# Kernel optimization log

Hardware: AMD Instinct MI355X
Metric: run time of the kernel (lower is better)

## Reference

```python
import jax, jax.numpy as jnp
import numpy as np

T, B = 128, 512
OBS_DIM = 512
HIDDEN = 512
ACTION_DIM = 18
LN_EPS = 1e-6  # flax LayerNorm default


def _layer_norm(x, scale, bias):
    m = jnp.mean(x, axis=-1, keepdims=True)
    v = jnp.var(x, axis=-1, keepdims=True)
    return (x - m) * jax.lax.rsqrt(v + LN_EPS) * scale + bias


def setup_inputs() -> dict:
    key = jax.random.key(0)
    ks = jax.random.split(key, 16)
    sc = lambda k, sh: jax.random.normal(k, sh, jnp.float32) * (1.0 / np.sqrt(sh[0]))
    d = {}
    d['hidden'] = jax.random.normal(ks[0], (B, HIDDEN), jnp.float32)
    d['obs'] = jax.random.normal(ks[1], (T, B, OBS_DIM), jnp.float32)
    d['dones'] = jax.random.randint(ks[2], (T, B), 0, 2).astype(bool)
    d['last_acts'] = jax.random.randint(ks[3], (T, B), 0, ACTION_DIM, dtype=jnp.int32)
    in0 = OBS_DIM + ACTION_DIM
    d['w0'] = sc(ks[4], (in0, HIDDEN)); d['b0'] = jnp.zeros((HIDDEN,), jnp.float32)
    d['ln0_s'] = jnp.ones((HIDDEN,), jnp.float32); d['ln0_b'] = jnp.zeros((HIDDEN,), jnp.float32)
    d['w1'] = sc(ks[5], (HIDDEN, HIDDEN)); d['b1'] = jnp.zeros((HIDDEN,), jnp.float32)
    d['ln1_s'] = jnp.ones((HIDDEN,), jnp.float32); d['ln1_b'] = jnp.zeros((HIDDEN,), jnp.float32)
    d['w_ir'] = sc(ks[6], (HIDDEN, HIDDEN)); d['b_ir'] = jnp.zeros((HIDDEN,), jnp.float32)
    d['w_iz'] = sc(ks[7], (HIDDEN, HIDDEN)); d['b_iz'] = jnp.zeros((HIDDEN,), jnp.float32)
    d['w_in'] = sc(ks[8], (HIDDEN, HIDDEN)); d['b_in'] = jnp.zeros((HIDDEN,), jnp.float32)
    d['w_hr'] = sc(ks[9], (HIDDEN, HIDDEN))
    d['w_hz'] = sc(ks[10], (HIDDEN, HIDDEN))
    d['w_hn'] = sc(ks[11], (HIDDEN, HIDDEN)); d['b_hn'] = jnp.zeros((HIDDEN,), jnp.float32)
    d['w_out'] = sc(ks[12], (HIDDEN, ACTION_DIM)); d['b_out'] = jnp.zeros((ACTION_DIM,), jnp.float32)
    return d


def reference(hidden, obs, dones, last_acts,
              w0, b0, ln0_s, ln0_b, w1, b1, ln1_s, ln1_b,
              w_ir, b_ir, w_iz, b_iz, w_in, b_in,
              w_hr, w_hz, w_hn, b_hn, w_out, b_out):
    # embed last actions and concat with obs: [T, B, obs_dim + action_dim]
    one_hot = jax.nn.one_hot(last_acts, ACTION_DIM, dtype=obs.dtype)
    x = jnp.concatenate([obs, one_hot], axis=-1)
    # MLP encoder: Dense -> LayerNorm -> relu, applied over all (T, B) at once
    x = jax.nn.relu(_layer_norm(x @ w0 + b0, ln0_s, ln0_b))
    x = jax.nn.relu(_layer_norm(x @ w1 + b1, ln1_s, ln1_b))

    # ScannedRNN: GRUCell with reset-to-zero carry on done, scanned over time
    def step(h, xs):
        xt, dt = xs  # xt: [B, H], dt: [B] bool
        h = jnp.where(dt[:, None], jnp.zeros_like(h), h)
        r = jax.nn.sigmoid(xt @ w_ir + b_ir + h @ w_hr)
        z = jax.nn.sigmoid(xt @ w_iz + b_iz + h @ w_hz)
        n = jnp.tanh(xt @ w_in + b_in + r * (h @ w_hn + b_hn))
        h_new = (1.0 - z) * n + z * h
        return h_new, h_new

    new_hidden, y = jax.lax.scan(step, hidden, (x, dones))
    q_vals = y @ w_out + b_out  # [T, B, action_dim]
    return new_hidden, q_vals
```

## Files before the change

kernel.cpp:

```cpp
#include <hip/hip_runtime.h>
#include <cstdint>
#include <cstddef>


#define TT 128
#define BBATCH 512
#define HH 512
#define MM 65536
#define AD 18

typedef __attribute__((ext_vector_type(8))) short short8;
typedef __attribute__((ext_vector_type(4))) float float4v;
typedef __attribute__((ext_vector_type(4))) unsigned int uint4v;

__device__ __forceinline__ unsigned short f2bf(float f) {
  union { float f; unsigned int u; } v; v.f = f;
  unsigned int r = v.u + 0x7fffu + ((v.u >> 16) & 1u);
  return (unsigned short)(r >> 16);
}
__device__ __forceinline__ float bf2f(unsigned short h) {
  union { unsigned int u; float f; } v; v.u = ((unsigned int)h) << 16;
  return v.f;
}

__device__ __forceinline__ unsigned int load_u32_coh(const unsigned int* p) {
  unsigned int v;
  asm volatile("global_load_dword %0, %1, off sc0 sc1\n\ts_waitcnt vmcnt(0)"
               : "=v"(v) : "v"(p) : "memory");
  return v;
}
__device__ __forceinline__ void store_u32_coh(unsigned int* p, unsigned int v) {
  asm volatile("global_store_dword %0, %1, off sc0 sc1"
               :: "v"(p), "v"(v) : "memory");
}
__device__ __forceinline__ void store_u16_coh(unsigned short* p, unsigned int v) {
  asm volatile("global_store_short %0, %1, off sc0 sc1"
               :: "v"(p), "v"(v) : "memory");
}

typedef __attribute__((address_space(3))) unsigned int* lds_u32p;
typedef const __attribute__((address_space(1))) unsigned int* glb_u32p;
__device__ __forceinline__ void async16(void* lds, const void* g) {
  __builtin_amdgcn_global_load_lds(
      (glb_u32p)(unsigned long long)g,
      (lds_u32p)(unsigned int)(unsigned long long)lds, 16, 0, 0);
}


__global__ __launch_bounds__(256) void k_conv_obs(
    const float* __restrict__ src, unsigned short* __restrict__ dst,
    unsigned int* __restrict__ flag) {
  if (blockIdx.x == 0 && threadIdx.x == 0) *flag = 0u;
  int i = blockIdx.x * 256 + threadIdx.x;
  float4v v = ((const float4v*)src)[i];
  unsigned long long pk = (unsigned long long)f2bf(v[0])
      | ((unsigned long long)f2bf(v[1]) << 16)
      | ((unsigned long long)f2bf(v[2]) << 32)
      | ((unsigned long long)f2bf(v[3]) << 48);
  ((unsigned long long*)dst)[i] = pk;
}

__global__ __launch_bounds__(256) void k_prep_t(
    const float* __restrict__ w0, const float* __restrict__ w1,
    const float* __restrict__ wir, const float* __restrict__ wiz,
    const float* __restrict__ win,
    unsigned short* __restrict__ W0at, unsigned short* __restrict__ W1t,
    unsigned short* __restrict__ Wit) {
  int o = blockIdx.x * 256 + threadIdx.x;
  int n = o >> 9, k = o & 511;
  int z = blockIdx.y;
  const float* s = (z == 0) ? w0 : (z == 1) ? w1 : (z == 2) ? wir
                 : (z == 3) ? wiz : win;
  unsigned short b = f2bf(s[k * 512 + n]);
  if (z == 0) W0at[o] = b;
  else if (z == 1) W1t[o] = b;
  else Wit[(size_t)(z - 2) * 262144 + o] = b;
}

__global__ __launch_bounds__(256) void k_prep_whf(
    const float* __restrict__ whr, const float* __restrict__ whz,
    const float* __restrict__ whn, unsigned short* __restrict__ Whf) {
  int i = blockIdx.x * 256 + threadIdx.x;
  int k = i / 1536, n = i - k * 1536;
  const float* s = (n < 512) ? whr : (n < 1024) ? whz : whn;
  float v = s[k * 512 + (n & 511)];
  Whf[((size_t)(k >> 3) * 1536 + n) * 8 + (k & 7)] = f2bf(v);
}

__global__ __launch_bounds__(256) void k_prep_misc(
    const float* __restrict__ w0, const float* __restrict__ bir,
    const float* __restrict__ biz, const float* __restrict__ bin,
    const float* __restrict__ wout, const float* __restrict__ hidden,
    const int* __restrict__ dI,
    unsigned short* __restrict__ w0act, float* __restrict__ gib,
    unsigned short* __restrict__ WoutT, unsigned short* __restrict__ hbuf,
    unsigned int* __restrict__ ready, unsigned int* __restrict__ flag) {
  int i = blockIdx.x * 256 + threadIdx.x;
  if (i < 9216) {
    int a = i >> 9, n = i & 511;
    w0act[i] = f2bf(w0[(512 + a) * 512 + n]);
  }
  if (i < 1536)
    gib[i] = (i < 512) ? bir[i] : (i < 1024) ? biz[i - 512] : bin[i - 1024];
  if (i < 32768) {
    int n = i >> 9, k = i & 511;
    WoutT[i] = f2bf(n < AD ? wout[k * AD + n] : 0.f);
  }
  if (i < 262144) hbuf[i] = f2bf(hidden[i]);
  if (i < 33280) ready[i] = 0u;
  if (i < 16384) { if (dI[i] & 0xFFFFFFFE) atomicOr(flag, 1u); }
}


template <int MODE>
__global__ __launch_bounds__(256) void k_gemm_bt(
    const unsigned short* __restrict__ Ab,
    const unsigned short* __restrict__ Btb,
    unsigned short* __restrict__ Cb,
    int Ndim, const float* __restrict__ bias,
    const unsigned short* __restrict__ gW,
    const int* __restrict__ acts) {
  __shared__ unsigned short As[4096];
  __shared__ unsigned short Bs[4096];
  const int tid = threadIdx.x, wave = tid >> 6, lane = tid & 63;
  const int quad = lane >> 4, l15 = lane & 15;
  const int m0 = blockIdx.x * 128, n0 = blockIdx.y * 128;
  const int mblk = (wave & 1) * 64, nblk = (wave >> 1) * 64;

  float4v acc[4][4];
#pragma unroll
  for (int a = 0; a < 4; ++a)
#pragma unroll
    for (int b = 0; b < 4; ++b) acc[a][b] = (float4v){0.f, 0.f, 0.f, 0.f};

  for (int k0 = 0; k0 < 512; k0 += 32) {
#pragma unroll
    for (int r = 0; r < 2; ++r) {
      int u = r * 256 + wave * 64 + lane;
      int ch = u >> 7, mm = u & 127;
      async16(&As[(size_t)(r * 256 + wave * 64) * 8],
              Ab + (size_t)(m0 + mm) * 512 + k0 + ch * 8);
      async16(&Bs[(size_t)(r * 256 + wave * 64) * 8],
              Btb + (size_t)(n0 + mm) * 512 + k0 + ch * 8);
    }
    __syncthreads();
    short8 afr[4], bfr[4];
#pragma unroll
    for (int mi = 0; mi < 4; ++mi)
      afr[mi] = *(const short8*)&As[((quad << 7) + mblk + mi * 16 + l15) * 8];
#pragma unroll
    for (int ni = 0; ni < 4; ++ni)
      bfr[ni] = *(const short8*)&Bs[((quad << 7) + nblk + ni * 16 + l15) * 8];
#pragma unroll
    for (int mi = 0; mi < 4; ++mi)
#pragma unroll
      for (int ni = 0; ni < 4; ++ni)
        acc[mi][ni] = __builtin_amdgcn_mfma_f32_16x16x32_bf16(
            afr[mi], bfr[ni], acc[mi][ni], 0, 0, 0);
    __syncthreads();
  }

#pragma unroll
  for (int mi = 0; mi < 4; ++mi) {
#pragma unroll
    for (int i = 0; i < 4; ++i) {
      int row = m0 + mblk + mi * 16 + quad * 4 + i;
      int arow = (MODE == 1) ? acts[row] : 0;
#pragma unroll
      for (int ni = 0; ni < 4; ++ni) {
        int col = n0 + nblk + ni * 16 + l15;
        float v = acc[mi][ni][i] + bias[col];
        if (MODE == 1) v += bf2f(gW[arow * 512 + col]);
        Cb[(size_t)row * Ndim + col] = f2bf(v);
      }
    }
  }
}


__global__ __launch_bounds__(256) void k_ln_relu(
    const unsigned short* __restrict__ X, unsigned short* __restrict__ Y,
    const float* __restrict__ sc, const float* __restrict__ bi) {
  int row = blockIdx.x * 4 + (threadIdx.x >> 6);
  int lane = threadIdx.x & 63;
  uint4v u = *(const uint4v*)(X + (size_t)row * 512 + lane * 8);
  float v[8];
#pragma unroll
  for (int j = 0; j < 4; ++j) {
    v[2 * j] = bf2f((unsigned short)(u[j] & 0xffffu));
    v[2 * j + 1] = bf2f((unsigned short)(u[j] >> 16));
  }
  float s = 0.f, q = 0.f;
#pragma unroll
  for (int j = 0; j < 8; ++j) { s += v[j]; q += v[j] * v[j]; }
#pragma unroll
  for (int d = 1; d < 64; d <<= 1) {
    s += __shfl_xor(s, d, 64);
    q += __shfl_xor(q, d, 64);
  }
  float mean = s * (1.f / 512.f);
  float var = fmaxf(q * (1.f / 512.f) - mean * mean, 0.f);
  float rstd = rsqrtf(var + 1e-6f);
  float4v s0 = *(const float4v*)(sc + lane * 8);
  float4v s1 = *(const float4v*)(sc + lane * 8 + 4);
  float4v c0 = *(const float4v*)(bi + lane * 8);
  float4v c1 = *(const float4v*)(bi + lane * 8 + 4);
  uint4v w;
#pragma unroll
  for (int j = 0; j < 4; ++j) {
    float a0 = fmaxf((v[2 * j] - mean) * rstd * (j < 2 ? s0[2 * j] : s1[2 * j - 4])
                         + (j < 2 ? c0[2 * j] : c1[2 * j - 4]), 0.f);
    float a1 = fmaxf((v[2 * j + 1] - mean) * rstd
                         * (j < 2 ? s0[2 * j + 1] : s1[2 * j - 3])
                         + (j < 2 ? c0[2 * j + 1] : c1[2 * j - 3]), 0.f);
    w[j] = (unsigned int)f2bf(a0) | ((unsigned int)f2bf(a1) << 16);
  }
  *(uint4v*)(Y + (size_t)row * 512 + lane * 8) = w;
}


__global__ __launch_bounds__(256, 1) void k_gru(
    const unsigned short* __restrict__ Whf, const unsigned short* __restrict__ gin,
    const float* __restrict__ bhn, const int* __restrict__ dI,
    const unsigned char* __restrict__ dB, const unsigned int* __restrict__ flag,
    const unsigned short* __restrict__ hbuf, unsigned short* __restrict__ ybuf,
    float* __restrict__ outh, unsigned int* __restrict__ ready) {
  const int tid = threadIdx.x, wave = tid >> 6, lane = tid & 63;
  const int quad = lane >> 4, l15 = lane & 15;
  const int rt = blockIdx.x & 7;
  const int cc = blockIdx.x >> 3;
  const int r0 = rt * 64 + wave * 16;
  const int col = cc * 16 + l15;
  const int bytemode = (int)(*flag);
  const float bhn_c = bhn[col];

  short8 bw[3][16];
#pragma unroll
  for (int kc = 0; kc < 16; ++kc)
#pragma unroll
    for (int g = 0; g < 3; ++g) {
      size_t u = (size_t)(kc * 4 + quad) * 1536 + (g * 512 + col);
      bw[g][kc] = *(const short8*)(Whf + u * 8);
    }

  float hprev[4];
#pragma unroll
  for (int i = 0; i < 4; ++i) {
    int row = r0 + quad * 4 + i;
    hprev[i] = bf2f(hbuf[(size_t)row * 512 + col]);
  }

  const int myrowA = r0 + l15;

  float ginr[4], ginz[4], ginn[4];
  int dd[4], dA;
  {
    const unsigned short* gbase = gin;
#pragma unroll
    for (int i = 0; i < 4; ++i) {
      int row = r0 + quad * 4 + i;
      dd[i] = bytemode ? (int)dB[row] : dI[row];
      ginr[i] = bf2f(gbase[(size_t)row * 1536 + col]);
      ginz[i] = bf2f(gbase[(size_t)row * 1536 + 512 + col]);
      ginn[i] = bf2f(gbase[(size_t)row * 1536 + 1024 + col]);
    }
    dA = bytemode ? (int)dB[myrowA] : dI[myrowA];
  }

  for (int t = 0; t < TT; ++t) {
    if (t > 0) {
      if (wave == 0) {
        const unsigned int* fp =
            ready + ((size_t)rt * 130 + t) * 32 + (lane & 31);
        unsigned int v;
        int guard = 0;
        do {
          v = load_u32_coh(fp);
        } while (__ballot(v == 0u) != 0ull && ++guard < (1 << 22));
      }
      __syncthreads();
      asm volatile("" ::: "memory");
    }

    const unsigned short* hsrc =
        (t == 0) ? hbuf : ybuf + (size_t)(t - 1) * 262144;
    const unsigned short* ap = hsrc + (size_t)myrowA * 512 + quad * 8;
    short8 af[16];
#pragma unroll
    for (int kc = 0; kc < 16; ++kc) af[kc] = *(const short8*)(ap + kc * 32);
    if (dA) {
      const short8 z8 = {0, 0, 0, 0, 0, 0, 0, 0};
#pragma unroll
      for (int kc = 0; kc < 16; ++kc) af[kc] = z8;
    }

    float4v a0 = {0.f, 0.f, 0.f, 0.f}, a1 = a0, a2 = a0;
#pragma unroll
    for (int kc = 0; kc < 16; ++kc) {
      a0 = __builtin_amdgcn_mfma_f32_16x16x32_bf16(af[kc], bw[0][kc], a0, 0, 0, 0);
      a1 = __builtin_amdgcn_mfma_f32_16x16x32_bf16(af[kc], bw[1][kc], a1, 0, 0, 0);
      a2 = __builtin_amdgcn_mfma_f32_16x16x32_bf16(af[kc], bw[2][kc], a2, 0, 0, 0);
    }

    unsigned short* ydst = ybuf + (size_t)t * 262144;
#pragma unroll
    for (int i = 0; i < 4; ++i) {
      int row = r0 + quad * 4 + i;
      float hold = dd[i] ? 0.f : hprev[i];
      float r = 1.f / (1.f + __expf(-(a0[i] + ginr[i])));
      float z = 1.f / (1.f + __expf(-(a1[i] + ginz[i])));
      float npre = ginn[i] + r * (a2[i] + bhn_c);
      float n = 1.f - 2.f / (1.f + __expf(2.f * npre));
      float hnew = (1.f - z) * n + z * hold;
      hprev[i] = hnew;
      store_u16_coh(ydst + (size_t)row * 512 + col, (unsigned int)f2bf(hnew));
      if (t == TT - 1) outh[(size_t)row * 512 + col] = hnew;
    }

    __syncthreads();
    if (tid == 0)
      store_u32_coh(&ready[((size_t)rt * 130 + t + 1) * 32 + cc], 1u);

    if (t < TT - 1) {
      int tn = t + 1;
      const unsigned short* gbase = gin + (size_t)tn * 512 * 1536;
#pragma unroll
      for (int i = 0; i < 4; ++i) {
        int row = r0 + quad * 4 + i;
        dd[i] = bytemode ? (int)dB[tn * 512 + row] : dI[tn * 512 + row];
        ginr[i] = bf2f(gbase[(size_t)row * 1536 + col]);
        ginz[i] = bf2f(gbase[(size_t)row * 1536 + 512 + col]);
        ginn[i] = bf2f(gbase[(size_t)row * 1536 + 1024 + col]);
      }
      dA = bytemode ? (int)dB[tn * 512 + myrowA] : dI[tn * 512 + myrowA];
    }
  }
}


__global__ __launch_bounds__(256) void k_qout(
    const unsigned short* __restrict__ Yb, const unsigned short* __restrict__ Wt,
    const float* __restrict__ bout, float* __restrict__ Q) {
  __shared__ unsigned short As[4096];
  __shared__ unsigned short Bs[2048];
  const int tid = threadIdx.x, wave = tid >> 6, lane = tid & 63;
  const int quad = lane >> 4, l15 = lane & 15;
  const int m0 = blockIdx.x * 128;

  float4v acc[2][4];
#pragma unroll
  for (int a = 0; a < 2; ++a)
#pragma unroll
    for (int b = 0; b < 4; ++b) acc[a][b] = (float4v){0.f, 0.f, 0.f, 0.f};

  for (int k0 = 0; k0 < 512; k0 += 32) {
#pragma unroll
    for (int r = 0; r < 2; ++r) {
      int u = r * 256 + wave * 64 + lane;
      int ch = u >> 7, mm = u & 127;
      async16(&As[(size_t)(r * 256 + wave * 64) * 8],
              Yb + (size_t)(m0 + mm) * 512 + k0 + ch * 8);
    }
    {
      int u = wave * 64 + lane;
      int ch = u >> 6, nn = u & 63;
      async16(&Bs[(size_t)(wave * 64) * 8], Wt + (size_t)nn * 512 + k0 + ch * 8);
    }
    __syncthreads();
    short8 afr[2], bfr[4];
#pragma unroll
    for (int mi = 0; mi < 2; ++mi)
      afr[mi] = *(const short8*)&As[((quad << 7) + wave * 32 + mi * 16 + l15) * 8];
#pragma unroll
    for (int ni = 0; ni < 4; ++ni)
      bfr[ni] = *(const short8*)&Bs[((quad << 6) + ni * 16 + l15) * 8];
#pragma unroll
    for (int mi = 0; mi < 2; ++mi)
#pragma unroll
      for (int ni = 0; ni < 4; ++ni)
        acc[mi][ni] = __builtin_amdgcn_mfma_f32_16x16x32_bf16(
            afr[mi], bfr[ni], acc[mi][ni], 0, 0, 0);
    __syncthreads();
  }
#pragma unroll
  for (int mi = 0; mi < 2; ++mi)
#pragma unroll
    for (int ni = 0; ni < 4; ++ni)
#pragma unroll
      for (int i = 0; i < 4; ++i) {
        int row = m0 + wave * 32 + mi * 16 + quad * 4 + i;
        int colq = ni * 16 + l15;
        if (colq < AD) Q[(size_t)row * AD + colq] = acc[mi][ni][i] + bout[colq];
      }
}


extern "C" void kernel_launch(void* const* d_in, const int* in_sizes, int n_in,
                              void* d_out, int out_size, void* d_ws,
                              size_t ws_size, hipStream_t stream) {
  const float* hidden = (const float*)d_in[0];
  const float* obs = (const float*)d_in[1];
  const void* dones = d_in[2];
  const int* acts = (const int*)d_in[3];
  const float* w0 = (const float*)d_in[4];
  const float* b0 = (const float*)d_in[5];
  const float* ln0s = (const float*)d_in[6];
  const float* ln0b = (const float*)d_in[7];
  const float* w1 = (const float*)d_in[8];
  const float* b1 = (const float*)d_in[9];
  const float* ln1s = (const float*)d_in[10];
  const float* ln1b = (const float*)d_in[11];
  const float* wir = (const float*)d_in[12];
  const float* bir = (const float*)d_in[13];
  const float* wiz = (const float*)d_in[14];
  const float* biz = (const float*)d_in[15];
  const float* win = (const float*)d_in[16];
  const float* bin = (const float*)d_in[17];
  const float* whr = (const float*)d_in[18];
  const float* whz = (const float*)d_in[19];
  const float* whn = (const float*)d_in[20];
  const float* bhn = (const float*)d_in[21];
  const float* wout = (const float*)d_in[22];
  const float* bout = (const float*)d_in[23];

  char* ws = (char*)d_ws;
  unsigned short* bufA = (unsigned short*)(ws);
  unsigned short* bufB = (unsigned short*)(ws + 67108864ULL);
  unsigned short* gin = (unsigned short*)(ws + 134217728ULL);
  char* D = ws + 134217728ULL + 201326592ULL;
  unsigned short* W0at = (unsigned short*)(D);
  unsigned short* W1t = (unsigned short*)(D + 524288);
  unsigned short* Wit = (unsigned short*)(D + 1048576);
  unsigned short* Whf = (unsigned short*)(D + 2621440);
  unsigned short* WoutT = (unsigned short*)(D + 4194304);
  unsigned short* w0act = (unsigned short*)(D + 4259840);
  float* gib = (float*)(D + 4292608);
  unsigned short* hbuf = (unsigned short*)(D + 4300800);
  unsigned int* ready = (unsigned int*)(D + 5349376);
  unsigned int* flag = ready + 33280;

  (void)in_sizes; (void)n_in; (void)out_size; (void)ws_size;

  k_conv_obs<<<32768, 256, 0, stream>>>(obs, bufA, flag);
  k_prep_t<<<dim3(1024, 5), 256, 0, stream>>>(w0, w1, wir, wiz, win, W0at, W1t, Wit);
  k_prep_whf<<<3072, 256, 0, stream>>>(whr, whz, whn, Whf);
  k_prep_misc<<<1024, 256, 0, stream>>>(w0, bir, biz, bin, wout, hidden,
                                        (const int*)dones, w0act, gib, WoutT,
                                        hbuf, ready, flag);
  k_gemm_bt<1><<<dim3(512, 4), 256, 0, stream>>>(bufA, W0at, bufB, 512, b0, w0act, acts);
  k_ln_relu<<<16384, 256, 0, stream>>>(bufB, bufA, ln0s, ln0b);
  k_gemm_bt<0><<<dim3(512, 4), 256, 0, stream>>>(bufA, W1t, bufB, 512, b1, nullptr, nullptr);
  k_ln_relu<<<16384, 256, 0, stream>>>(bufB, bufA, ln1s, ln1b);
  k_gemm_bt<0><<<dim3(512, 12), 256, 0, stream>>>(bufA, Wit, gin, 1536, gib, nullptr, nullptr);
  k_gru<<<256, 256, 0, stream>>>(Whf, gin, bhn, (const int*)dones,
                                 (const unsigned char*)dones, flag, hbuf, bufB,
                                 (float*)d_out, ready);
  k_qout<<<512, 256, 0, stream>>>(bufB, WoutT, bout, (float*)d_out + 262144);
}
```

Baseline: 1.361 ms.

## Restructure GRU scan to 32 column blocks with per-wave row-group flags

The recurrent kernel now launches 32 blocks, one per 16-column slice, instead of 256. Each wave handles two 64-row groups and processes four 16-row tiles per group. The block-wide __syncthreads barrier is replaced by per-wave polling of ready flags for each row group, and a group's ready flag is published only after the stores from its previous step are drained. The goal is to cut cross-block synchronisation and let waves proceed independently, at the cost of much less parallelism (32 CUs) and more serial MFMA work per wave for each timestep.

```diff
diff --git a/kernel.cpp b/kernel.cpp
--- a/kernel.cpp
+++ b/kernel.cpp
@@ -36,6 +36,9 @@
 __device__ __forceinline__ void store_u16_coh(unsigned short* p, unsigned int v) {
   asm volatile("global_store_short %0, %1, off sc0 sc1"
                :: "v"(p), "v"(v) : "memory");
+}
+__device__ __forceinline__ void drain_vmem() {
+  asm volatile("s_waitcnt vmcnt(0)" ::: "memory");
 }
 
 typedef __attribute__((address_space(3))) unsigned int* lds_u32p;
@@ -227,9 +230,7 @@
     float* __restrict__ outh, unsigned int* __restrict__ ready) {
   const int tid = threadIdx.x, wave = tid >> 6, lane = tid & 63;
   const int quad = lane >> 4, l15 = lane & 15;
-  const int rt = blockIdx.x & 7;
-  const int cc = blockIdx.x >> 3;
-  const int r0 = rt * 64 + wave * 16;
+  const int cc = blockIdx.x;
   const int col = cc * 16 + l15;
   const int bytemode = (int)(*flag);
   const float bhn_c = bhn[col];
@@ -243,96 +244,92 @@
       bw[g][kc] = *(const short8*)(Whf + u * 8);
     }
 
-  float hprev[4];
-#pragma unroll
-  for (int i = 0; i < 4; ++i) {
-    int row = r0 + quad * 4 + i;
-    hprev[i] = bf2f(hbuf[(size_t)row * 512 + col]);
-  }
-
-  const int myrowA = r0 + l15;
-
-  float ginr[4], ginz[4], ginn[4];
-  int dd[4], dA;
-  {
-    const unsigned short* gbase = gin;
-#pragma unroll
-    for (int i = 0; i < 4; ++i) {
-      int row = r0 + quad * 4 + i;
-      dd[i] = bytemode ? (int)dB[row] : dI[row];
-      ginr[i] = bf2f(gbase[(size_t)row * 1536 + col]);
-      ginz[i] = bf2f(gbase[(size_t)row * 1536 + 512 + col]);
-      ginn[i] = bf2f(gbase[(size_t)row * 1536 + 1024 + col]);
-    }
-    dA = bytemode ? (int)dB[myrowA] : dI[myrowA];
-  }
-
+  float hold[2][16];
+#pragma unroll
+  for (int s = 0; s < 2; ++s) {
+    int g = wave + s * 4;
+#pragma unroll
+    for (int tile = 0; tile < 4; ++tile)
+#pragma unroll
+      for (int i = 0; i < 4; ++i) {
+        int row = g * 64 + tile * 16 + quad * 4 + i;
+        hold[s][tile * 4 + i] = bf2f(hbuf[(size_t)row * 512 + col]);
+      }
+  }
+
+  int pg = -1, pt = 0;
   for (int t = 0; t < TT; ++t) {
-    if (t > 0) {
-      if (wave == 0) {
+#pragma unroll
+    for (int s = 0; s < 2; ++s) {
+      const int g = wave + s * 4;
+      if (t > 0) {
         const unsigned int* fp =
-            ready + ((size_t)rt * 130 + t) * 32 + (lane & 31);
+            ready + ((size_t)g * 130 + t) * 32 + (lane & 31);
         unsigned int v;
         int guard = 0;
         do {
           v = load_u32_coh(fp);
-        } while (__ballot(v == 0u) != 0ull && ++guard < (1 << 22));
+        } while (__ballot(v == 0u) != 0ull && ++guard < (1 << 20));
       }
-      __syncthreads();
-      asm volatile("" ::: "memory");
-    }
-
-    const unsigned short* hsrc =
-        (t == 0) ? hbuf : ybuf + (size_t)(t - 1) * 262144;
-    const unsigned short* ap = hsrc + (size_t)myrowA * 512 + quad * 8;
-    short8 af[16];
-#pragma unroll
-    for (int kc = 0; kc < 16; ++kc) af[kc] = *(const short8*)(ap + kc * 32);
-    if (dA) {
-      const short8 z8 = {0, 0, 0, 0, 0, 0, 0, 0};
-#pragma unroll
-      for (int kc = 0; kc < 16; ++kc) af[kc] = z8;
-    }
-
-    float4v a0 = {0.f, 0.f, 0.f, 0.f}, a1 = a0, a2 = a0;
-#pragma unroll
-    for (int kc = 0; kc < 16; ++kc) {
-      a0 = __builtin_amdgcn_mfma_f32_16x16x32_bf16(af[kc], bw[0][kc], a0, 0, 0, 0);
-      a1 = __builtin_amdgcn_mfma_f32_16x16x32_bf16(af[kc], bw[1][kc], a1, 0, 0, 0);
-      a2 = __builtin_amdgcn_mfma_f32_16x16x32_bf16(af[kc], bw[2][kc], a2, 0, 0, 0);
-    }
-
-    unsigned short* ydst = ybuf + (size_t)t * 262144;
-#pragma unroll
-    for (int i = 0; i < 4; ++i) {
-      int row = r0 + quad * 4 + i;
-      float hold = dd[i] ? 0.f : hprev[i];
-      float r = 1.f / (1.f + __expf(-(a0[i] + ginr[i])));
-      float z = 1.f / (1.f + __expf(-(a1[i] + ginz[i])));
-      float npre = ginn[i] + r * (a2[i] + bhn_c);
-      float n = 1.f - 2.f / (1.f + __expf(2.f * npre));
-      float hnew = (1.f - z) * n + z * hold;
-      hprev[i] = hnew;
-      store_u16_coh(ydst + (size_t)row * 512 + col, (unsigned int)f2bf(hnew));
-      if (t == TT - 1) outh[(size_t)row * 512 + col] = hnew;
-    }
-
-    __syncthreads();
-    if (tid == 0)
-      store_u32_coh(&ready[((size_t)rt * 130 + t + 1) * 32 + cc], 1u);
-
-    if (t < TT - 1) {
-      int tn = t + 1;
-      const unsigned short* gbase = gin + (size_t)tn * 512 * 1536;
-#pragma unroll
-      for (int i = 0; i < 4; ++i) {
-        int row = r0 + quad * 4 + i;
-        dd[i] = bytemode ? (int)dB[tn * 512 + row] : dI[tn * 512 + row];
-        ginr[i] = bf2f(gbase[(size_t)row * 1536 + col]);
-        ginz[i] = bf2f(gbase[(size_t)row * 1536 + 512 + col]);
-        ginn[i] = bf2f(gbase[(size_t)row * 1536 + 1024 + col]);
+      const unsigned short* hsrc =
+          (t == 0) ? hbuf : ybuf + (size_t)(t - 1) * 262144;
+      unsigned short* ydst = ybuf + (size_t)t * 262144;
+      const unsigned short* gbase = gin + (size_t)t * 512 * 1536;
+
+#pragma unroll
+      for (int tile = 0; tile < 4; ++tile) {
+        const int rowA = g * 64 + tile * 16 + l15;
+        int dA = bytemode ? (int)dB[t * 512 + rowA] : dI[t * 512 + rowA];
+        const unsigned short* ap = hsrc + (size_t)rowA * 512 + quad * 8;
+        short8 af[16];
+#pragma unroll
+        for (int kc = 0; kc < 16; ++kc) af[kc] = *(const short8*)(ap + kc * 32);
+        if (dA) {
+          const short8 z8 = {0, 0, 0, 0, 0, 0, 0, 0};
+#pragma unroll
+          for (int kc = 0; kc < 16; ++kc) af[kc] = z8;
+        }
+        float ginr[4], ginz[4], ginn[4];
+        int dd[4];
+#pragma unroll
+        for (int i = 0; i < 4; ++i) {
+          int row = g * 64 + tile * 16 + quad * 4 + i;
+          dd[i] = bytemode ? (int)dB[t * 512 + row] : dI[t * 512 + row];
+          ginr[i] = bf2f(gbase[(size_t)row * 1536 + col]);
+          ginz[i] = bf2f(gbase[(size_t)row * 1536 + 512 + col]);
+          ginn[i] = bf2f(gbase[(size_t)row * 1536 + 1024 + col]);
+        }
+
+        float4v a0 = {0.f, 0.f, 0.f, 0.f}, a1 = a0, a2 = a0;
+#pragma unroll
+        for (int kc = 0; kc < 16; ++kc) {
+          a0 = __builtin_amdgcn_mfma_f32_16x16x32_bf16(af[kc], bw[0][kc], a0, 0, 0, 0);
+          a1 = __builtin_amdgcn_mfma_f32_16x16x32_bf16(af[kc], bw[1][kc], a1, 0, 0, 0);
+          a2 = __builtin_amdgcn_mfma_f32_16x16x32_bf16(af[kc], bw[2][kc], a2, 0, 0, 0);
+        }
+
+        if (tile == 0) {
+          drain_vmem();
+          if (pg >= 0 && lane == 0)
+            store_u32_coh(&ready[((size_t)pg * 130 + pt + 1) * 32 + cc], 1u);
+        }
+
+#pragma unroll
+        for (int i = 0; i < 4; ++i) {
+          int row = g * 64 + tile * 16 + quad * 4 + i;
+          float holdv = dd[i] ? 0.f : hold[s][tile * 4 + i];
+          float r = 1.f / (1.f + __expf(-(a0[i] + ginr[i])));
+          float z = 1.f / (1.f + __expf(-(a1[i] + ginz[i])));
+          float npre = ginn[i] + r * (a2[i] + bhn_c);
+          float n = 1.f - 2.f / (1.f + __expf(2.f * npre));
+          float hnew = (1.f - z) * n + z * holdv;
+          hold[s][tile * 4 + i] = hnew;
+          store_u16_coh(ydst + (size_t)row * 512 + col,
+                        (unsigned int)f2bf(hnew));
+          if (t == TT - 1) outh[(size_t)row * 512 + col] = hnew;
+        }
       }
-      dA = bytemode ? (int)dB[tn * 512 + myrowA] : dI[tn * 512 + myrowA];
+      pg = g; pt = t;
     }
   }
 }
@@ -452,8 +449,8 @@
   k_gemm_bt<0><<<dim3(512, 4), 256, 0, stream>>>(bufA, W1t, bufB, 512, b1, nullptr, nullptr);
   k_ln_relu<<<16384, 256, 0, stream>>>(bufB, bufA, ln1s, ln1b);
   k_gemm_bt<0><<<dim3(512, 12), 256, 0, stream>>>(bufA, Wit, gin, 1536, gib, nullptr, nullptr);
-  k_gru<<<256, 256, 0, stream>>>(Whf, gin, bhn, (const int*)dones,
-                                 (const unsigned char*)dones, flag, hbuf, bufB,
-                                 (float*)d_out, ready);
+  k_gru<<<32, 256, 0, stream>>>(Whf, gin, bhn, (const int*)dones,
+                                (const unsigned char*)dones, flag, hbuf, bufB,
+                                (float*)d_out, ready);
   k_qout<<<512, 256, 0, stream>>>(bufB, WoutT, bout, (float*)d_out + 262144);
 }
```

After: 4.103 ms. +201.4%, slower.
